# Optimization experiments

Measured on AMD Instinct MI355X. Metric: run time of the kernel, lower is better.

The kernel has to match this reference:

```python
import jax, jax.numpy as jnp
import numpy as np

NUM_HEADS = 32
NUM_KV_HEADS = 8
HEAD_DIM = 128
SCALE = 1.0 / np.sqrt(HEAD_DIM)
LENGTHS = np.array([1024, 768, 512, 896], dtype=np.int32)  # ragged prefill lengths


def setup_inputs() -> dict:
    key = jax.random.key(0)
    kq, kk, kv = jax.random.split(key, 3)
    total = int(LENGTHS.sum())  # 3200
    q = jax.random.normal(kq, (total, NUM_HEADS * HEAD_DIM), dtype=jnp.float32)
    k = jax.random.normal(kk, (total, NUM_KV_HEADS * HEAD_DIM), dtype=jnp.float32)
    v = jax.random.normal(kv, (total, NUM_KV_HEADS * HEAD_DIM), dtype=jnp.float32)
    cu = jnp.asarray(np.concatenate([[0], np.cumsum(LENGTHS)]), dtype=jnp.int32)
    return {"q": q, "k": k, "v": v, "cu_seqlens": cu, "max_seqlen": 1024}


def _varlen_attn(q, k, v, cu_seqlens, max_seqlen):
    # q: [T, H*D], k/v: [T, KVH*D]; cu_seqlens: [B+1]
    T = q.shape[0]
    B = cu_seqlens.shape[0] - 1
    S = max_seqlen
    q = q.reshape(T, NUM_HEADS, HEAD_DIM)
    k = k.reshape(T, NUM_KV_HEADS, HEAD_DIM)
    v = v.reshape(T, NUM_KV_HEADS, HEAD_DIM)

    tok = jnp.arange(T, dtype=jnp.int32)
    batch_id = jnp.searchsorted(cu_seqlens[1:], tok, side="right").astype(jnp.int32)
    pos = tok - cu_seqlens[batch_id]

    # pad to [B, S, h, d] (zeros beyond each sequence, like _varlen_to_padded)
    qp = jnp.zeros((B, S, NUM_HEADS, HEAD_DIM), q.dtype).at[batch_id, pos].set(q)
    kp = jnp.zeros((B, S, NUM_KV_HEADS, HEAD_DIM), k.dtype).at[batch_id, pos].set(k)
    vp = jnp.zeros((B, S, NUM_KV_HEADS, HEAD_DIM), v.dtype).at[batch_id, pos].set(v)

    # GQA: repeat_interleave kv heads to match q heads
    rep = NUM_HEADS // NUM_KV_HEADS
    kp = jnp.repeat(kp, rep, axis=2)
    vp = jnp.repeat(vp, rep, axis=2)

    scores = jnp.einsum("bqhd,bkhd->bhqk", qp, kp) * SCALE
    # causal mask only (matches torch SDPA is_causal=True on padded input;
    # with equal q/k lengths, padded keys are never attended by valid queries)
    qi = jnp.arange(S)[:, None]
    kj = jnp.arange(S)[None, :]
    scores = jnp.where(kj <= qi, scores, jnp.finfo(scores.dtype).min)
    attn = jax.nn.softmax(scores, axis=-1)
    outp = jnp.einsum("bhqk,bkhd->bqhd", attn, vp)

    # unpad back to varlen and flatten heads
    out = outp[batch_id, pos]  # [T, H, D]
    return out.reshape(T, NUM_HEADS * HEAD_DIM)


def reference(q, k, v, cu_seqlens, max_seqlen):
    return _varlen_attn(q, k, v, cu_seqlens, max_seqlen)
```

## Files before the change

kernel.cpp:

```cpp
#include <hip/hip_runtime.h>
#include <hip/hip_bf16.h>

#define NH 32
#define NKVH 8
#define HD 128
#define KT 64
#define QT 32

typedef __attribute__((ext_vector_type(8))) __bf16 bf16x8;
typedef __attribute__((ext_vector_type(4))) short s16x4;
typedef __attribute__((ext_vector_type(4))) float f32x4;
typedef __attribute__((ext_vector_type(2))) unsigned int u32x2;
typedef __attribute__((ext_vector_type(4))) unsigned int u32x4;

__device__ inline unsigned short f2bf(float f) {
    unsigned int u = __builtin_bit_cast(unsigned int, f);
    u += 0x7fffu + ((u >> 16) & 1u);
    return (unsigned short)(u >> 16);
}
__device__ inline unsigned int pk2(float lo, float hi) {
    return (unsigned int)f2bf(lo) | ((unsigned int)f2bf(hi) << 16);
}
__device__ inline f32x4 mfma16(bf16x8 a, bf16x8 b, f32x4 c) {
    return __builtin_amdgcn_mfma_f32_16x16x32_bf16(a, b, c, 0, 0, 0);
}
__device__ inline f32x4 mfma16k16(s16x4 a, s16x4 b, f32x4 c) {
#if __has_builtin(__builtin_amdgcn_mfma_f32_16x16x16bf16_1k)
    return __builtin_amdgcn_mfma_f32_16x16x16bf16_1k(a, b, c, 0, 0, 0);
#else
    f32x4 d = c;
    asm volatile("v_mfma_f32_16x16x16_bf16 %0, %1, %2, %0"
                 : "+v"(d) : "v"(a), "v"(b));
    return d;
#endif
}
__device__ inline void async16(unsigned short* lds, const unsigned short* g) {
    __builtin_amdgcn_global_load_lds(
        (const __attribute__((address_space(1))) unsigned int*)g,
        (__attribute__((address_space(3))) unsigned int*)lds, 16, 0, 0);
}

__global__ __launch_bounds__(256) void prep_kv(const float* __restrict__ kg,
                                               const float* __restrict__ vg,
                                               const int* __restrict__ cu,
                                               unsigned short* __restrict__ kb,
                                               unsigned short* __restrict__ vt,
                                               int* __restrict__ ctr) {
    const int b = blockIdx.y, kvh = blockIdx.z;
    if (blockIdx.x == 0 && b == 0 && kvh == 0 && threadIdx.x == 0) *ctr = 0;
    const int bstart = cu[b];
    const int L = cu[b + 1] - bstart;
    const int kv0 = blockIdx.x * 64;
    if (kv0 >= L) return;
    const int tid = threadIdx.x;
    const int wid = tid >> 6, lane = tid & 63;
    __shared__ __align__(16) unsigned short Vl[HD * 64];

    #pragma unroll
    for (int it = 0; it < 4; ++it) {
        int jp = wid * 8 + (lane >> 3);
        int c4 = (lane & 7) + it * 8;
        int j0 = jp * 2;
        int jj0 = kv0 + j0;
        f32x4 va = f32x4{0.f, 0.f, 0.f, 0.f}, vb = f32x4{0.f, 0.f, 0.f, 0.f};
        if (jj0 < L)     va = *(const f32x4*)&vg[(size_t)(bstart + jj0) * (NKVH * HD) + kvh * HD + c4 * 4];
        if (jj0 + 1 < L) vb = *(const f32x4*)&vg[(size_t)(bstart + jj0 + 1) * (NKVH * HD) + kvh * HD + c4 * 4];
        #pragma unroll
        for (int i = 0; i < 4; ++i) {
            int d = c4 * 4 + i;
            int idx = (d * 64 + j0) ^ ((d & 7) << 3);
            *(unsigned int*)&Vl[idx] = pk2(va[i], vb[i]);
        }
    }

    #pragma unroll
    for (int it = 0; it < 4; ++it) {
        int u = tid + it * 256;
        int j = u >> 4, c8 = u & 15;
        int jj = kv0 + j;
        if (jj < L) {
            const float* p = &kg[(size_t)(bstart + jj) * (NKVH * HD) + kvh * HD + c8 * 8];
            f32x4 a = *(const f32x4*)p;
            f32x4 bq = *(const f32x4*)(p + 4);
            u32x4 r = {pk2(a[0], a[1]), pk2(a[2], a[3]), pk2(bq[0], bq[1]), pk2(bq[2], bq[3])};
            *(u32x4*)&kb[(size_t)(bstart + jj) * (NKVH * HD) + kvh * HD + c8 * 8] = r;
        }
    }
    __syncthreads();

    const size_t vtb = (size_t)bstart * (NKVH * HD) + (size_t)kvh * HD * L;
    #pragma unroll
    for (int it = 0; it < 8; ++it) {
        int u = tid + it * 256;
        int d = u >> 4, c = u & 15;
        int j0 = c * 4;
        if (kv0 + j0 >= L) continue;
        int idx = d * 64 + (j0 ^ ((d & 7) << 3));
        u32x2 w = *(const u32x2*)&Vl[idx];
        *(u32x2*)&vt[vtb + (size_t)d * L + kv0 + j0] = w;
    }
}

__global__ __launch_bounds__(256, 2) void fa14(const float* __restrict__ qg,
                                               const unsigned short* __restrict__ kb,
                                               const unsigned short* __restrict__ vt,
                                               const int* __restrict__ cu,
                                               float* __restrict__ outg,
                                               int* __restrict__ ctr, int B) {
    const int tid = threadIdx.x;
    const int wid = tid >> 6, lane = tid & 63;
    const int lg = lane >> 4, lr = lane & 15;

    __shared__ __align__(16) unsigned short Klds[2][KT * HD];
    __shared__ __align__(16) unsigned short Vlds[2][HD * KT];
    __shared__ int s_item;

    int totalF = 0;
    {
        int prev = cu[0];
        #pragma unroll 1
        for (int bb = 0; bb < B; ++bb) {
            int nxt = cu[bb + 1];
            totalF += (nxt - prev + QT - 1) / QT;
            prev = nxt;
        }
    }
    const int totalItems = totalF * NKVH;
    const float scv = 0.08838834764831843f * 1.4426950408889634f;

    for (;;) {
        if (tid == 0) s_item = atomicAdd(ctr, 1);
        __syncthreads();
        const int item = s_item;
        if (item >= totalItems) return;

        const int kvh = item / totalF;
        const int f = item - kvh * totalF;
        int rem = f, bstart = 0, L = 0, nqf = 0, found = 0;
        int prev = cu[0];
        #pragma unroll 1
        for (int bb = 0; bb < B; ++bb) {
            int nxt = cu[bb + 1];
            int len = nxt - prev;
            int nq = (len + QT - 1) / QT;
            if (!found) {
                if (rem < nq) { bstart = prev; L = len; nqf = nq; found = 1; }
                else rem -= nq;
            }
            prev = nxt;
        }
        const int qt = nqf - 1 - rem;
        const int q0 = qt * QT;
        const int h = kvh * 4 + wid;

        bf16x8 qf0[4], qf1[4];
        #pragma unroll
        for (int kk = 0; kk < 4; ++kk) {
            int row0 = q0 + lr;
            int tok0 = bstart + (row0 < L ? row0 : L - 1);
            const float* p = &qg[(size_t)tok0 * (NH * HD) + h * HD + kk * 32 + lg * 8];
            f32x4 a = *(const f32x4*)p;
            f32x4 bq = *(const f32x4*)(p + 4);
            u32x4 r = {pk2(a[0] * scv, a[1] * scv), pk2(a[2] * scv, a[3] * scv),
                       pk2(bq[0] * scv, bq[1] * scv), pk2(bq[2] * scv, bq[3] * scv)};
            qf0[kk] = __builtin_bit_cast(bf16x8, r);
        }
        #pragma unroll
        for (int kk = 0; kk < 4; ++kk) {
            int row1 = q0 + 16 + lr;
            int tok1 = bstart + (row1 < L ? row1 : L - 1);
            const float* p = &qg[(size_t)tok1 * (NH * HD) + h * HD + kk * 32 + lg * 8];
            f32x4 a = *(const f32x4*)p;
            f32x4 bq = *(const f32x4*)(p + 4);
            u32x4 r = {pk2(a[0] * scv, a[1] * scv), pk2(a[2] * scv, a[3] * scv),
                       pk2(bq[0] * scv, bq[1] * scv), pk2(bq[2] * scv, bq[3] * scv)};
            qf1[kk] = __builtin_bit_cast(bf16x8, r);
        }

        f32x4 acc0[8], acc1[8];
        #pragma unroll
        for (int i = 0; i < 8; ++i) {
            acc0[i] = f32x4{0.f, 0.f, 0.f, 0.f};
            acc1[i] = f32x4{0.f, 0.f, 0.f, 0.f};
        }
        float lsum0 = 0.f, lsum1 = 0.f;

        const int ntiles = (q0 + QT + KT - 1) / KT;
        const unsigned short* kbase = kb + (size_t)bstart * (NKVH * HD) + kvh * HD;
        const unsigned short* vbase = vt + (size_t)bstart * (NKVH * HD) + (size_t)kvh * HD * L;

        auto STAGE = [&](int buf, int kv0) {
            unsigned short* Kd = Klds[buf];
            unsigned short* Vd = Vlds[buf];
            #pragma unroll
            for (int i = 0; i < 4; ++i) {
                int U = i * 256 + tid;
                int j = U >> 4, u = U & 15;
                int up = (u & 8) | ((u ^ j) & 7);
                int jj = kv0 + j; if (jj >= L) jj = L - 1;
                async16(Kd + (size_t)U * 8, kbase + (size_t)jj * (NKVH * HD) + up * 8);
            }
            #pragma unroll
            for (int i = 0; i < 4; ++i) {
                int U = i * 256 + tid;
                int d = U >> 3, u = U & 7;
                int up = u ^ (d & 7);
                int col = kv0 + up * 8;
                if (col > L - 8) col = L - 8;
                async16(Vd + (size_t)U * 8, vbase + (size_t)d * L + col);
            }
        };

        STAGE(0, 0);
        __syncthreads();

        for (int kt = 0; kt < ntiles; ++kt) {
            const int kv0 = kt * KT;
            const int buf = kt & 1;
            if (kt + 1 < ntiles) STAGE(buf ^ 1, kv0 + KT);

            const unsigned short* Kc = Klds[buf];
            const unsigned short* Vc = Vlds[buf];

            const int shi_raw = ((q0 + QT - 1 - kv0) >> 4) + 1;
            const int s_hi = shi_raw < 4 ? shi_raw : 4;
            const bool needmask = (kv0 + KT - 1) > q0;
            const int qpos0 = q0 + lr;
            const int qpos1 = q0 + 16 + lr;

            f32x4 st0[4], st1[4];
            __builtin_amdgcn_s_setprio(1);
            #pragma unroll
            for (int s = 0; s < 4; ++s) {
                if (s < s_hi) {
                    f32x4 a0 = f32x4{0.f, 0.f, 0.f, 0.f};
                    f32x4 a1 = f32x4{0.f, 0.f, 0.f, 0.f};
                    int row = s * 16 + lr;
                    #pragma unroll
                    for (int kk = 0; kk < 4; ++kk) {
                        int un = kk * 4 + lg;
                        int cs = ((un & 8) | ((un ^ row) & 7)) * 8;
                        bf16x8 kf = *(const bf16x8*)&Kc[row * HD + cs];
                        a0 = mfma16(kf, qf0[kk], a0);
                        a1 = mfma16(kf, qf1[kk], a1);
                    }
                    st0[s] = a0;
                    st1[s] = a1;
                }
            }
            __builtin_amdgcn_s_setprio(0);

            #pragma unroll
            for (int s = 0; s < 4; ++s) {
                if (s < s_hi) {
                    #pragma unroll
                    for (int r = 0; r < 4; ++r) {
                        int j = kv0 + s * 16 + lg * 4 + r;
                        float p0 = __builtin_amdgcn_exp2f(st0[s][r]);
                        float p1 = __builtin_amdgcn_exp2f(st1[s][r]);
                        p0 = (needmask && j > qpos0) ? 0.f : p0;
                        p1 = (needmask && j > qpos1) ? 0.f : p1;
                        st0[s][r] = p0;
                        st1[s][r] = p1;
                        lsum0 += p0;
                        lsum1 += p1;
                    }
                }
            }

            #pragma unroll
            for (int s = 0; s < 4; ++s) {
                if (s < s_hi) {
                    u32x2 pp0 = {pk2(st0[s][0], st0[s][1]), pk2(st0[s][2], st0[s][3])};
                    u32x2 pp1 = {pk2(st1[s][0], st1[s][1]), pk2(st1[s][2], st1[s][3])};
                    s16x4 pb0 = __builtin_bit_cast(s16x4, pp0);
                    s16x4 pb1 = __builtin_bit_cast(s16x4, pp1);
                    __builtin_amdgcn_s_setprio(1);
                    #pragma unroll
                    for (int dsb = 0; dsb < 8; ++dsb) {
                        int vrow = dsb * 16 + lr;
                        int c0 = (s * 16 + lg * 4) ^ ((vrow & 7) << 3);
                        s16x4 vf = *(const s16x4*)&Vc[vrow * 64 + c0];
                        acc0[dsb] = mfma16k16(vf, pb0, acc0[dsb]);
                        acc1[dsb] = mfma16k16(vf, pb1, acc1[dsb]);
                    }
                    __builtin_amdgcn_s_setprio(0);
                }
            }
            __syncthreads();
        }

        {
            float l = lsum0;
            l += __shfl_xor(l, 16);
            l += __shfl_xor(l, 32);
            int q = q0 + lr;
            if (q < L) {
                float inv = 1.0f / l;
                size_t base = (size_t)(bstart + q) * (NH * HD) + h * HD;
                #pragma unroll
                for (int dsb = 0; dsb < 8; ++dsb) {
                    f32x4 o = acc0[dsb] * inv;
                    *(f32x4*)&outg[base + dsb * 16 + lg * 4] = o;
                }
            }
        }
        {
            float l = lsum1;
            l += __shfl_xor(l, 16);
            l += __shfl_xor(l, 32);
            int q = q0 + 16 + lr;
            if (q < L) {
                float inv = 1.0f / l;
                size_t base = (size_t)(bstart + q) * (NH * HD) + h * HD;
                #pragma unroll
                for (int dsb = 0; dsb < 8; ++dsb) {
                    f32x4 o = acc1[dsb] * inv;
                    *(f32x4*)&outg[base + dsb * 16 + lg * 4] = o;
                }
            }
        }
    }
}

extern "C" void kernel_launch(void* const* d_in, const int* in_sizes, int n_in,
                              void* d_out, int out_size, void* d_ws, size_t ws_size,
                              hipStream_t stream) {
    const float* q = (const float*)d_in[0];
    const float* k = (const float*)d_in[1];
    const float* v = (const float*)d_in[2];
    const int* cu  = (const int*)d_in[3];
    int T = in_sizes[0] / (NH * HD);
    int B = in_sizes[3] - 1;

    unsigned short* kb = (unsigned short*)d_ws;
    unsigned short* vt = kb + (size_t)T * (NKVH * HD);
    int* ctr = (int*)(vt + (size_t)T * (NKVH * HD));

    dim3 gkv((T + 63) / 64, B, NKVH);
    prep_kv<<<gkv, 256, 0, stream>>>(k, v, cu, kb, vt, ctr);

    fa14<<<dim3(512), dim3(256), 0, stream>>>(q, kb, vt, cu, (float*)d_out, ctr, B);
}
```

Baseline: 88.89 us.

## Drop LDS staging and schedule work per wave, reading K/V from global

Removes the double-buffered LDS staging of K and V tiles and the block-level barriers. Each wave now grabs its own work item (one query head per item) through a per-wave atomic counter, and it reads K and V fragments directly from global memory, relying on the cache. This removes barrier stalls and the dependency on the other waves in the block, but it gives up sharing each K/V tile across the four heads of a KV group. It also issues many more small global loads with uncoalesced strides for V.

```diff
diff --git a/kernel.cpp b/kernel.cpp
--- a/kernel.cpp
+++ b/kernel.cpp
@@ -33,11 +33,6 @@
                  : "+v"(d) : "v"(a), "v"(b));
     return d;
 #endif
-}
-__device__ inline void async16(unsigned short* lds, const unsigned short* g) {
-    __builtin_amdgcn_global_load_lds(
-        (const __attribute__((address_space(1))) unsigned int*)g,
-        (__attribute__((address_space(3))) unsigned int*)lds, 16, 0, 0);
 }
 
 __global__ __launch_bounds__(256) void prep_kv(const float* __restrict__ kg,
@@ -101,19 +96,14 @@
     }
 }
 
-__global__ __launch_bounds__(256, 2) void fa14(const float* __restrict__ qg,
+__global__ __launch_bounds__(256, 2) void fa15(const float* __restrict__ qg,
                                                const unsigned short* __restrict__ kb,
                                                const unsigned short* __restrict__ vt,
                                                const int* __restrict__ cu,
                                                float* __restrict__ outg,
                                                int* __restrict__ ctr, int B) {
-    const int tid = threadIdx.x;
-    const int wid = tid >> 6, lane = tid & 63;
+    const int lane = threadIdx.x & 63;
     const int lg = lane >> 4, lr = lane & 15;
-
-    __shared__ __align__(16) unsigned short Klds[2][KT * HD];
-    __shared__ __align__(16) unsigned short Vlds[2][HD * KT];
-    __shared__ int s_item;
 
     int totalF = 0;
     {
@@ -125,17 +115,19 @@
             prev = nxt;
         }
     }
-    const int totalItems = totalF * NKVH;
+    const int totalItems = totalF * NH;
     const float scv = 0.08838834764831843f * 1.4426950408889634f;
 
     for (;;) {
-        if (tid == 0) s_item = atomicAdd(ctr, 1);
-        __syncthreads();
-        const int item = s_item;
+        int item;
+        if (lane == 0) item = atomicAdd(ctr, 1);
+        item = __shfl(item, 0);
         if (item >= totalItems) return;
 
-        const int kvh = item / totalF;
-        const int f = item - kvh * totalF;
+        const int grp = item >> 2, hsub = item & 3;
+        const int kvh = grp / totalF;
+        const int f = grp - kvh * totalF;
+        const int h = kvh * 4 + hsub;
         int rem = f, bstart = 0, L = 0, nqf = 0, found = 0;
         int prev = cu[0];
         #pragma unroll 1
@@ -151,7 +143,6 @@
         }
         const int qt = nqf - 1 - rem;
         const int q0 = qt * QT;
-        const int h = kvh * 4 + wid;
 
         bf16x8 qf0[4], qf1[4];
         #pragma unroll
@@ -189,38 +180,8 @@
         const unsigned short* kbase = kb + (size_t)bstart * (NKVH * HD) + kvh * HD;
         const unsigned short* vbase = vt + (size_t)bstart * (NKVH * HD) + (size_t)kvh * HD * L;
 
-        auto STAGE = [&](int buf, int kv0) {
-            unsigned short* Kd = Klds[buf];
-            unsigned short* Vd = Vlds[buf];
-            #pragma unroll
-            for (int i = 0; i < 4; ++i) {
-                int U = i * 256 + tid;
-                int j = U >> 4, u = U & 15;
-                int up = (u & 8) | ((u ^ j) & 7);
-                int jj = kv0 + j; if (jj >= L) jj = L - 1;
-                async16(Kd + (size_t)U * 8, kbase + (size_t)jj * (NKVH * HD) + up * 8);
-            }
-            #pragma unroll
-            for (int i = 0; i < 4; ++i) {
-                int U = i * 256 + tid;
-                int d = U >> 3, u = U & 7;
-                int up = u ^ (d & 7);
-                int col = kv0 + up * 8;
-                if (col > L - 8) col = L - 8;
-                async16(Vd + (size_t)U * 8, vbase + (size_t)d * L + col);
-            }
-        };
-
-        STAGE(0, 0);
-        __syncthreads();
-
         for (int kt = 0; kt < ntiles; ++kt) {
             const int kv0 = kt * KT;
-            const int buf = kt & 1;
-            if (kt + 1 < ntiles) STAGE(buf ^ 1, kv0 + KT);
-
-            const unsigned short* Kc = Klds[buf];
-            const unsigned short* Vc = Vlds[buf];
 
             const int shi_raw = ((q0 + QT - 1 - kv0) >> 4) + 1;
             const int s_hi = shi_raw < 4 ? shi_raw : 4;
@@ -229,26 +190,26 @@
             const int qpos1 = q0 + 16 + lr;
 
             f32x4 st0[4], st1[4];
-            __builtin_amdgcn_s_setprio(1);
             #pragma unroll
             for (int s = 0; s < 4; ++s) {
                 if (s < s_hi) {
                     f32x4 a0 = f32x4{0.f, 0.f, 0.f, 0.f};
                     f32x4 a1 = f32x4{0.f, 0.f, 0.f, 0.f};
-                    int row = s * 16 + lr;
+                    int jj = kv0 + s * 16 + lr;
+                    int jtok = jj < L ? jj : L - 1;
+                    const unsigned short* kp = kbase + (size_t)jtok * (NKVH * HD) + lg * 8;
+                    __builtin_amdgcn_s_setprio(1);
                     #pragma unroll
                     for (int kk = 0; kk < 4; ++kk) {
-                        int un = kk * 4 + lg;
-                        int cs = ((un & 8) | ((un ^ row) & 7)) * 8;
-                        bf16x8 kf = *(const bf16x8*)&Kc[row * HD + cs];
+                        bf16x8 kf = *(const bf16x8*)(kp + kk * 32);
                         a0 = mfma16(kf, qf0[kk], a0);
                         a1 = mfma16(kf, qf1[kk], a1);
                     }
+                    __builtin_amdgcn_s_setprio(0);
                     st0[s] = a0;
                     st1[s] = a1;
                 }
             }
-            __builtin_amdgcn_s_setprio(0);
 
             #pragma unroll
             for (int s = 0; s < 4; ++s) {
@@ -275,19 +236,18 @@
                     u32x2 pp1 = {pk2(st1[s][0], st1[s][1]), pk2(st1[s][2], st1[s][3])};
                     s16x4 pb0 = __builtin_bit_cast(s16x4, pp0);
                     s16x4 pb1 = __builtin_bit_cast(s16x4, pp1);
+                    const unsigned short* vp = vbase + kv0 + s * 16 + lg * 4;
                     __builtin_amdgcn_s_setprio(1);
                     #pragma unroll
                     for (int dsb = 0; dsb < 8; ++dsb) {
                         int vrow = dsb * 16 + lr;
-                        int c0 = (s * 16 + lg * 4) ^ ((vrow & 7) << 3);
-                        s16x4 vf = *(const s16x4*)&Vc[vrow * 64 + c0];
+                        s16x4 vf = *(const s16x4*)(vp + (size_t)vrow * L);
                         acc0[dsb] = mfma16k16(vf, pb0, acc0[dsb]);
                         acc1[dsb] = mfma16k16(vf, pb1, acc1[dsb]);
                     }
                     __builtin_amdgcn_s_setprio(0);
                 }
             }
-            __syncthreads();
         }
 
         {
@@ -340,5 +300,5 @@
     dim3 gkv((T + 63) / 64, B, NKVH);
     prep_kv<<<gkv, 256, 0, stream>>>(k, v, cu, kb, vt, ctr);
 
-    fa14<<<dim3(512), dim3(256), 0, stream>>>(q, kb, vt, cu, (float*)d_out, ctr, B);
-}
+    fa15<<<dim3(512), dim3(256), 0, stream>>>(q, kb, vt, cu, (float*)d_out, ctr, B);
+}
```

Measured after the change: 233.1 us. 2.62x slower.
